# Kernel optimization log

Measured on AMD Instinct MI355X. Metric: run time of the kernel, lower is better.

## Reference

```python
import jax, jax.numpy as jnp
import numpy as np

D_MODEL = 1024
NUM_HEADS = 16
HEAD_SIZE = D_MODEL // NUM_HEADS
THETA = 10000.0
MAX_SEQ_LEN = 4096


def _rope_tables():
    # (max_seq_len, head_size//2) cos/sin tables, matching RotaryPositionalEmbedding
    k = jnp.arange(HEAD_SIZE // 2, dtype=jnp.float32)
    inv_freq = 1.0 / (THETA ** (2.0 * k / HEAD_SIZE))
    pos = jnp.arange(MAX_SEQ_LEN, dtype=jnp.float32)
    ang = pos[:, None] * inv_freq[None, :]
    return jnp.cos(ang), jnp.sin(ang)


def _apply_rope(x, cos, sin):
    # x: (b, h, s, d); cos/sin: (s, d//2) -> broadcast over (b, h)
    x1 = x[..., ::2]
    x2 = x[..., 1::2]
    out_even = x1 * cos - x2 * sin
    out_odd = x2 * cos + x1 * sin
    # re-interleave pairs back to (..., d)
    return jnp.stack([out_even, out_odd], axis=-1).reshape(x.shape)


def setup_inputs() -> dict:
    key = jax.random.key(0)
    k1, k2, k3 = jax.random.split(key, 3)
    b, s = 1, 4096
    std_qkv = np.sqrt(2.0 / (D_MODEL + 3 * D_MODEL))
    std_o = np.sqrt(2.0 / (D_MODEL + D_MODEL))
    return {
        "x": jax.random.normal(k1, (b, s, D_MODEL), dtype=jnp.float32),
        "token_positions": jnp.arange(s, dtype=jnp.int32),
        "W_qkv": jax.random.normal(k2, (3 * D_MODEL, D_MODEL), dtype=jnp.float32) * std_qkv,
        "W_o": jax.random.normal(k3, (D_MODEL, D_MODEL), dtype=jnp.float32) * std_o,
    }


def reference(x, token_positions, W_qkv, W_o):
    b, s, _ = x.shape
    qkv = jnp.einsum("bsd,ed->bse", x, W_qkv)  # (b, s, 3*d_model)
    q, k, v = jnp.split(qkv, 3, axis=-1)

    def to_heads(t):
        return t.reshape(b, s, NUM_HEADS, HEAD_SIZE).transpose(0, 2, 1, 3)  # (b, h, s, hs)

    q, k, v = to_heads(q), to_heads(k), to_heads(v)

    cos_tab, sin_tab = _rope_tables()
    cos = cos_tab[token_positions]  # (s, hs//2)
    sin = sin_tab[token_positions]
    q = _apply_rope(q, cos, sin)
    k = _apply_rope(k, cos, sin)

    scale = 1.0 / jnp.sqrt(jnp.asarray(HEAD_SIZE, dtype=x.dtype))
    scores = jnp.einsum("bhqd,bhkd->bhqk", q, k) * scale  # (b, h, s, s)
    causal = jnp.tril(jnp.ones((s, s), dtype=bool))
    scores = jnp.where(causal, scores, jnp.finfo(scores.dtype).min)
    attn = jax.nn.softmax(scores, axis=-1)
    out = jnp.einsum("bhqk,bhkd->bhqd", attn, v)  # (b, h, s, hs)
    out = out.transpose(0, 2, 1, 3).reshape(b, s, D_MODEL)
    return jnp.einsum("bsd,ed->bse", out, W_o)
```

## Files before the change

### kernel.cpp

```cpp
#include <hip/hip_runtime.h>
#include <stdint.h>

typedef unsigned short u16;
typedef __attribute__((ext_vector_type(8))) short bf16x8;
typedef __attribute__((ext_vector_type(4))) float f32x4;

#define LN_THETA 9.210340371976184f
#define SLEN 4096
#define DMODEL 1024

__device__ __forceinline__ u16 f2bf(float f) {
  union { float f; unsigned u; } v; v.f = f;
  unsigned u = v.u;
  return (u16)((u + 0x7FFFu + ((u >> 16) & 1u)) >> 16);
}
__device__ __forceinline__ u16 f2bf_trunc(float f) {
  union { float f; unsigned u; } v; v.f = f;
  return (u16)(v.u >> 16);
}
__device__ __forceinline__ float bf2f(u16 b) {
  union { unsigned u; float f; } v; v.u = ((unsigned)b) << 16;
  return v.f;
}
__device__ __forceinline__ float fexp2(float x) {
#if __has_builtin(__builtin_amdgcn_exp2f)
  return __builtin_amdgcn_exp2f(x);
#else
  return exp2f(x);
#endif
}

__device__ __forceinline__ f32x4 mfma16(bf16x8 a, bf16x8 b, f32x4 c) {
  return __builtin_amdgcn_mfma_f32_16x16x32_bf16(a, b, c, 0, 0, 0);
}

__device__ __forceinline__ void async16(const u16* g, u16* l) {
  __builtin_amdgcn_global_load_lds(
      (const __attribute__((address_space(1))) unsigned int*)g,
      (__attribute__((address_space(3))) unsigned int*)l, 16, 0, 0);
}

__global__ void prep_kernel(const int* __restrict__ tokpos,
                            float2* __restrict__ tab,
                            const float* __restrict__ x,
                            const float* __restrict__ wqkv,
                            const float* __restrict__ wo,
                            u16* __restrict__ xb, u16* __restrict__ wqkvb,
                            u16* __restrict__ wob) {
  if (blockIdx.x < 512) {
    int t = blockIdx.x * 256 + threadIdx.x;
    int s = t >> 5, i = t & 31;
    float inv = expf(-(float)(2 * i) * (LN_THETA / 64.0f));
    float ang = (float)tokpos[s] * inv;
    float sn, cs;
    sincosf(ang, &sn, &cs);
    tab[t] = make_float2(cs, sn);
    return;
  }
  int i = (blockIdx.x - 512) * 256 + threadIdx.x;
  const float* src;
  u16* dst;
  if (i < (1 << 20)) {
    src = x; dst = xb;
  } else if (i < (1 << 20) + (3 << 18)) {
    i -= (1 << 20); src = wqkv; dst = wqkvb;
  } else {
    i -= (1 << 20) + (3 << 18); src = wo; dst = wob;
  }
  float4 v = ((const float4*)src)[i];
  ushort4 o;
  o.x = f2bf(v.x); o.y = f2bf(v.y); o.z = f2bf(v.z); o.w = f2bf(v.w);
  ((ushort4*)dst)[i] = o;
}

__global__ __launch_bounds__(256) void gemm_qkv_kernel(
    const u16* __restrict__ A, const u16* __restrict__ B,
    u16* __restrict__ qb, u16* __restrict__ kb,
    u16* __restrict__ vbT, const float2* __restrict__ cstab) {
  const int K = 1024;
  __shared__ __align__(16) char smem[128 * 136 * 2];
  u16 (*As)[64] = (u16(*)[64])smem;
  u16 (*Bs)[64] = (u16(*)[64])(smem + 16384);
  u16 (*Ts)[136] = (u16(*)[136])smem;
  const int tid = threadIdx.x;
  const int wave = tid >> 6, lane = tid & 63;
  const int quad = lane >> 4, col = lane & 15;
  const int rowBase = blockIdx.x * 128;
  const int colBase = blockIdx.y * 128;
  const int wm = (wave >> 1) * 64, wn = (wave & 1) * 64;

  const int sr8 = lane >> 3;
  const int sseg = ((lane & 7) ^ sr8) * 8;
  const u16* gA = A + (size_t)(rowBase + wave * 8 + sr8) * K + sseg;
  const u16* gB = B + (size_t)(colBase + wave * 8 + sr8) * K + sseg;
  u16* ldsA = &As[wave * 8 + sr8][(lane & 7) * 8];
  u16* ldsB = &Bs[wave * 8 + sr8][(lane & 7) * 8];

  const int segh[2] = {((quad ^ (col & 7)) * 8), (((4 + quad) ^ (col & 7)) * 8)};

  f32x4 acc[4][4];
#pragma unroll
  for (int i = 0; i < 4; ++i)
#pragma unroll
    for (int j = 0; j < 4; ++j)
      acc[i][j] = f32x4{0.f, 0.f, 0.f, 0.f};

  for (int kk = 0; kk < K; kk += 64) {
    __syncthreads();
#pragma unroll
    for (int j = 0; j < 4; ++j) {
      async16(gA + (size_t)j * 32 * K + kk, ldsA + j * 32 * 64);
      async16(gB + (size_t)j * 32 * K + kk, ldsB + j * 32 * 64);
    }
    __syncthreads();
#pragma unroll
    for (int h = 0; h < 2; ++h) {
      bf16x8 af[4], bfr[4];
#pragma unroll
      for (int i = 0; i < 4; ++i)
        af[i] = *(const bf16x8*)&As[wm + i * 16 + col][segh[h]];
#pragma unroll
      for (int j = 0; j < 4; ++j)
        bfr[j] = *(const bf16x8*)&Bs[wn + j * 16 + col][segh[h]];
#pragma unroll
      for (int i = 0; i < 4; ++i)
#pragma unroll
        for (int j = 0; j < 4; ++j)
          acc[i][j] = mfma16(af[i], bfr[j], acc[i][j]);
    }
  }
  __syncthreads();

  const int sec = rowBase >> 10;

  if (sec < 2) {
    const float qs = (sec == 0) ? 0.125f * 1.4426950408889634f : 1.0f;
#pragma unroll
    for (int j = 0; j < 4; ++j) {
      int sl = wn + j * 16 + col;
      int s = colBase + sl;
#pragma unroll
      for (int i = 0; i < 4; ++i) {
        int el = wm + i * 16 + quad * 4;
        int d = (rowBase + el) & 63;
        float v0 = acc[i][j][0], v1 = acc[i][j][1];
        float v2 = acc[i][j][2], v3 = acc[i][j][3];
        float2 cs0 = cstab[s * 32 + (d >> 1)];
        float2 cs1 = cstab[s * 32 + (d >> 1) + 1];
        ushort4 pk;
        pk.x = f2bf(qs * (v0 * cs0.x - v1 * cs0.y));
        pk.y = f2bf(qs * (v1 * cs0.x + v0 * cs0.y));
        pk.z = f2bf(qs * (v2 * cs1.x - v3 * cs1.y));
        pk.w = f2bf(qs * (v3 * cs1.x + v2 * cs1.y));
        *(ushort4*)&Ts[sl][el] = pk;
      }
    }
    __syncthreads();
    int sl = tid >> 1, hf = tid & 1;
    int hh = ((rowBase & 1023) >> 6) + hf;
    u16* dst = (sec == 0 ? qb : kb) + ((size_t)hh * SLEN + colBase + sl) * 64;
    const u16* srcp = &Ts[sl][hf * 64];
#pragma unroll
    for (int kq = 0; kq < 8; ++kq)
      ((int4*)dst)[kq] = ((const int4*)srcp)[kq];
  } else {
#pragma unroll
    for (int j = 0; j < 4; ++j) {
      int sl = wn + j * 16 + col;
#pragma unroll
      for (int i = 0; i < 4; ++i) {
        int el = wm + i * 16 + quad * 4;
#pragma unroll
        for (int r = 0; r < 4; ++r)
          Ts[el + r][sl] = f2bf(acc[i][j][r]);
      }
    }
    __syncthreads();
    int el = tid >> 1, sh = tid & 1;
    int e = rowBase - 2048 + el;
    int hh = e >> 6, d = e & 63;
    u16* dst = vbT + (size_t)(hh * 64 + d) * SLEN + colBase + sh * 64;
    const u16* srcp = &Ts[el][sh * 64];
#pragma unroll
    for (int kq = 0; kq < 8; ++kq)
      ((int4*)dst)[kq] = ((const int4*)srcp)[kq];
  }
}

__global__ __launch_bounds__(256) void gemm_out_kernel(
    const u16* __restrict__ A, const u16* __restrict__ B,
    float* __restrict__ outf) {
  const int K = 1024;
  __shared__ __align__(16) u16 As[128][64];
  __shared__ __align__(16) u16 Bs[64][64];
  const int tid = threadIdx.x;
  const int wave = tid >> 6, lane = tid & 63;
  const int quad = lane >> 4, col = lane & 15;
  const int rowBase = blockIdx.x * 128;
  const int colBase = blockIdx.y * 64;

  const int sr8 = lane >> 3;
  const int sseg = ((lane & 7) ^ sr8) * 8;
  const u16* gA = A + (size_t)(rowBase + wave * 8 + sr8) * K + sseg;
  const u16* gB = B + (size_t)(colBase + wave * 8 + sr8) * K + sseg;
  u16* ldsA = &As[wave * 8 + sr8][(lane & 7) * 8];
  u16* ldsB = &Bs[wave * 8 + sr8][(lane & 7) * 8];

  const int segh[2] = {((quad ^ (col & 7)) * 8), (((4 + quad) ^ (col & 7)) * 8)};

  f32x4 acc[2][4];
#pragma unroll
  for (int i = 0; i < 2; ++i)
#pragma unroll
    for (int j = 0; j < 4; ++j)
      acc[i][j] = f32x4{0.f, 0.f, 0.f, 0.f};

  for (int kk = 0; kk < K; kk += 64) {
    __syncthreads();
#pragma unroll
    for (int j = 0; j < 4; ++j)
      async16(gA + (size_t)j * 32 * K + kk, ldsA + j * 32 * 64);
#pragma unroll
    for (int j = 0; j < 2; ++j)
      async16(gB + (size_t)j * 32 * K + kk, ldsB + j * 32 * 64);
    __syncthreads();
#pragma unroll
    for (int h = 0; h < 2; ++h) {
      bf16x8 af[2], bfr[4];
#pragma unroll
      for (int i = 0; i < 2; ++i)
        af[i] = *(const bf16x8*)&As[wave * 32 + i * 16 + col][segh[h]];
#pragma unroll
      for (int j = 0; j < 4; ++j)
        bfr[j] = *(const bf16x8*)&Bs[j * 16 + col][segh[h]];
#pragma unroll
      for (int i = 0; i < 2; ++i)
#pragma unroll
        for (int j = 0; j < 4; ++j)
          acc[i][j] = mfma16(af[i], bfr[j], acc[i][j]);
    }
  }

#pragma unroll
  for (int i = 0; i < 2; ++i) {
    int r0 = rowBase + wave * 32 + i * 16 + quad * 4;
#pragma unroll
    for (int j = 0; j < 4; ++j) {
      int cc = colBase + j * 16 + col;
#pragma unroll
      for (int r = 0; r < 4; ++r)
        outf[(size_t)(r0 + r) * DMODEL + cc] = acc[i][j][r];
    }
  }
}

__global__ __launch_bounds__(256) void flash_kernel(
    const u16* __restrict__ qbuf, const u16* __restrict__ kbuf,
    const u16* __restrict__ vbT, u16* __restrict__ po,
    float* __restrict__ pl) {
  const int S = SLEN;
  const int h = blockIdx.x;
  const int y = blockIdx.y;
  int tile, c0, c1;
  if (y < 32) {
    tile = 32 + y; c0 = 0; c1 = 31;
  } else {
    int k = (y - 32) >> 1;
    if ((y - 32) & 1) { tile = 31 - k; c0 = 0; c1 = tile; }
    else { tile = 63 - k; c0 = 32; c1 = tile; }
  }
  const int id = (tile < 32) ? tile : (32 + 2 * (tile - 32) + (c0 ? 1 : 0));

  const int wave = threadIdx.x >> 6, lane = threadIdx.x & 63;
  const int quad = lane >> 4, col = lane & 15;
  const u16* Q = qbuf + (size_t)h * S * 64;
  const u16* Kh = kbuf + (size_t)h * S * 64;
  const u16* Vt = vbT + (size_t)h * 64 * S;

  __shared__ __align__(16) u16 Ks[64][64];
  __shared__ __align__(16) u16 Vs[64][64];
  __shared__ __align__(16) u16 Pld[4][16][72];

  const int sr = lane >> 3;
  const int sw = ((lane & 7) ^ sr) * 8;
  const int dcol = (lane & 7) * 8;
  const int segA = ((quad ^ (col & 7)) * 8);
  const int segB = (((quad ^ 4) ^ (col & 7)) * 8);

  const int qrow0 = tile * 64 + wave * 16;

  bf16x8 qf0, qf1;
  {
    const u16* qp = &Q[(size_t)(qrow0 + col) * 64 + quad * 8];
    qf0 = *(const bf16x8*)qp;
    qf1 = *(const bf16x8*)(qp + 32);
  }

  const bf16x8 ones = {(short)0x3F80, (short)0x3F80, (short)0x3F80,
                       (short)0x3F80, (short)0x3F80, (short)0x3F80,
                       (short)0x3F80, (short)0x3F80};

  f32x4 o[4], lacc;
#pragma unroll
  for (int n = 0; n < 4; ++n) o[n] = f32x4{0.f, 0.f, 0.f, 0.f};
  lacc = f32x4{0.f, 0.f, 0.f, 0.f};

  for (int c = c0; c <= c1; ++c) {
    const int k0 = c * 64;
    __syncthreads();
    {
#pragma unroll
      for (int t = 0; t < 2; ++t) {
        int row = wave * 16 + t * 8 + sr;
        async16(Kh + (size_t)(k0 + row) * 64 + sw, &Ks[row][dcol]);
        async16(Vt + (size_t)row * S + k0 + sw, &Vs[row][dcol]);
      }
    }
    __syncthreads();

    bf16x8 kf0[4], kf1[4], vf0[4], vf1[4];
#pragma unroll
    for (int j = 0; j < 4; ++j) {
      kf0[j] = *(const bf16x8*)&Ks[16 * j + col][segA];
      kf1[j] = *(const bf16x8*)&Ks[16 * j + col][segB];
    }
#pragma unroll
    for (int n = 0; n < 4; ++n) {
      vf0[n] = *(const bf16x8*)&Vs[16 * n + col][segA];
      vf1[n] = *(const bf16x8*)&Vs[16 * n + col][segB];
    }
    const bool lastc = (c == tile);
    f32x4 s[4];
#pragma unroll
    for (int j = 0; j < 4; ++j)
      s[j] = mfma16(qf1, kf1[j],
                    mfma16(qf0, kf0[j], f32x4{0.f, 0.f, 0.f, 0.f}));
    float p[4][4];
#pragma unroll
    for (int r = 0; r < 4; ++r) {
      const int qabs = qrow0 + quad * 4 + r;
#pragma unroll
      for (int j = 0; j < 4; ++j) {
        float e = fexp2(s[j][r]);
        if (lastc && (k0 + 16 * j + col > qabs)) e = 0.f;
        p[j][r] = e;
      }
    }
#pragma unroll
    for (int j = 0; j < 4; ++j)
#pragma unroll
      for (int r = 0; r < 4; ++r)
        Pld[wave][quad * 4 + r][16 * j + col] = f2bf_trunc(p[j][r]);
    bf16x8 pa0 = *(const bf16x8*)&Pld[wave][col][quad * 8];
    bf16x8 pa1 = *(const bf16x8*)&Pld[wave][col][quad * 8 + 32];
    lacc = mfma16(pa1, ones, mfma16(pa0, ones, lacc));
#pragma unroll
    for (int n = 0; n < 4; ++n)
      o[n] = mfma16(pa1, vf1[n], mfma16(pa0, vf0[n], o[n]));
  }

  u16* pob = po + (((size_t)h * 96 + id) * 64) * 64;
  float* plb = pl + ((size_t)h * 96 + id) * 64;
#pragma unroll
  for (int r = 0; r < 4; ++r) {
    int rowl = wave * 16 + quad * 4 + r;
    u16* dst = pob + (size_t)rowl * 64 + col;
#pragma unroll
    for (int n = 0; n < 4; ++n) dst[16 * n] = f2bf(o[n][r]);
    if (col == 0) plb[rowl] = lacc[r];
  }
}

__global__ __launch_bounds__(256) void reduce_kernel(
    const u16* __restrict__ po, const float* __restrict__ pl,
    u16* __restrict__ attn) {
  const int h = blockIdx.x, tile = blockIdx.y;
  const int tid = threadIdx.x;
  const int row = tid >> 2, dg = (tid & 3) * 16;
  int id0, ns;
  if (tile < 32) { id0 = tile; ns = 1; }
  else { id0 = 32 + 2 * (tile - 32); ns = 2; }

  float acc[16];
#pragma unroll
  for (int q = 0; q < 16; ++q) acc[q] = 0.f;
  float l = 0.f;
  for (int s = 0; s < ns; ++s) {
    const size_t base = ((size_t)h * 96 + id0 + s) * 64;
    const u16* p = po + (base + row) * 64 + dg;
    l += pl[base + row];
#pragma unroll
    for (int q = 0; q < 16; ++q) acc[q] += bf2f(p[q]);
  }
  float inv = 1.0f / l;
  u16* dst = attn + (size_t)(tile * 64 + row) * DMODEL + h * 64 + dg;
  ushort4 o0, o1, o2, o3;
  o0.x = f2bf(acc[0] * inv);  o0.y = f2bf(acc[1] * inv);
  o0.z = f2bf(acc[2] * inv);  o0.w = f2bf(acc[3] * inv);
  o1.x = f2bf(acc[4] * inv);  o1.y = f2bf(acc[5] * inv);
  o1.z = f2bf(acc[6] * inv);  o1.w = f2bf(acc[7] * inv);
  o2.x = f2bf(acc[8] * inv);  o2.y = f2bf(acc[9] * inv);
  o2.z = f2bf(acc[10] * inv); o2.w = f2bf(acc[11] * inv);
  o3.x = f2bf(acc[12] * inv); o3.y = f2bf(acc[13] * inv);
  o3.z = f2bf(acc[14] * inv); o3.w = f2bf(acc[15] * inv);
  ((ushort4*)dst)[0] = o0; ((ushort4*)dst)[1] = o1;
  ((ushort4*)dst)[2] = o2; ((ushort4*)dst)[3] = o3;
}

extern "C" void kernel_launch(void* const* d_in, const int* in_sizes, int n_in,
                              void* d_out, int out_size, void* d_ws,
                              size_t ws_size, hipStream_t stream) {
  const float* x = (const float*)d_in[0];
  const int* tokpos = (const int*)d_in[1];
  const float* wqkv = (const float*)d_in[2];
  const float* wo = (const float*)d_in[3];
  float* out = (float*)d_out;

  char* ws = (char*)d_ws;
  u16* xb    = (u16*)(ws);
  u16* wqkvb = (u16*)(ws + ((size_t)8 << 20));
  u16* wob   = (u16*)(ws + ((size_t)14 << 20));
  u16* qb    = (u16*)(ws + ((size_t)16 << 20));
  u16* kb    = (u16*)(ws + ((size_t)24 << 20));
  u16* vbT   = (u16*)(ws + ((size_t)32 << 20));
  u16* attn  = (u16*)(ws + ((size_t)40 << 20));
  float2* cstab = (float2*)(ws + ((size_t)48 << 20));
  u16* po    = (u16*)(ws);
  float* pl  = (float*)(ws + ((size_t)13 << 20));

  prep_kernel<<<dim3(8704), dim3(256), 0, stream>>>(tokpos, cstab, x, wqkv, wo,
                                                    xb, wqkvb, wob);
  gemm_qkv_kernel<<<dim3(24, 32), dim3(256), 0, stream>>>(
      wqkvb, xb, qb, kb, vbT, cstab);
  flash_kernel<<<dim3(16, 96), dim3(256), 0, stream>>>(qb, kb, vbT, po, pl);
  reduce_kernel<<<dim3(16, 64), dim3(256), 0, stream>>>(po, pl, attn);
  gemm_out_kernel<<<dim3(32, 16), dim3(256), 0, stream>>>(attn, wob, out);
}
```

Before: 210.4 us.

## Shrink GEMM tiles for more blocks and transpose flash scores for packed P stores

Both GEMM kernels switch to smaller output tiles (QKV 128x64, out-projection 64x64) and double their grids, so more blocks run across the CUs and each thread holds fewer registers. The flash kernel computes scores transposed (K times Q), so each lane holds consecutive keys for one query row. It can then write P to LDS as packed bf16 pairs using a byte-permute instead of scattered 16-bit stores. The smaller tiles lower per-block data reuse and add global traffic in exchange for more parallelism.

```diff
diff --git a/kernel.cpp b/kernel.cpp
--- a/kernel.cpp
+++ b/kernel.cpp
@@ -13,10 +13,6 @@
   union { float f; unsigned u; } v; v.f = f;
   unsigned u = v.u;
   return (u16)((u + 0x7FFFu + ((u >> 16) & 1u)) >> 16);
-}
-__device__ __forceinline__ u16 f2bf_trunc(float f) {
-  union { float f; unsigned u; } v; v.f = f;
-  return (u16)(v.u >> 16);
 }
 __device__ __forceinline__ float bf2f(u16 b) {
   union { unsigned u; float f; } v; v.u = ((unsigned)b) << 16;
@@ -27,6 +23,15 @@
   return __builtin_amdgcn_exp2f(x);
 #else
   return exp2f(x);
+#endif
+}
+__device__ __forceinline__ unsigned pack_bf16_trunc(float lo, float hi) {
+  union { float f; unsigned u; } a, b;
+  a.f = hi; b.f = lo;
+#if __has_builtin(__builtin_amdgcn_perm)
+  return __builtin_amdgcn_perm(a.u, b.u, 0x07060302u);
+#else
+  return (a.u & 0xffff0000u) | (b.u >> 16);
 #endif
 }
 
@@ -78,16 +83,17 @@
     u16* __restrict__ qb, u16* __restrict__ kb,
     u16* __restrict__ vbT, const float2* __restrict__ cstab) {
   const int K = 1024;
-  __shared__ __align__(16) char smem[128 * 136 * 2];
+  __shared__ __align__(16) char smem[24576];
   u16 (*As)[64] = (u16(*)[64])smem;
   u16 (*Bs)[64] = (u16(*)[64])(smem + 16384);
   u16 (*Ts)[136] = (u16(*)[136])smem;
+  u16 (*Tv)[72]  = (u16(*)[72])smem;
   const int tid = threadIdx.x;
   const int wave = tid >> 6, lane = tid & 63;
   const int quad = lane >> 4, col = lane & 15;
   const int rowBase = blockIdx.x * 128;
-  const int colBase = blockIdx.y * 128;
-  const int wm = (wave >> 1) * 64, wn = (wave & 1) * 64;
+  const int colBase = blockIdx.y * 64;
+  const int wm = wave * 32;
 
   const int sr8 = lane >> 3;
   const int sseg = ((lane & 7) ^ sr8) * 8;
@@ -98,9 +104,9 @@
 
   const int segh[2] = {((quad ^ (col & 7)) * 8), (((4 + quad) ^ (col & 7)) * 8)};
 
-  f32x4 acc[4][4];
-#pragma unroll
-  for (int i = 0; i < 4; ++i)
+  f32x4 acc[2][4];
+#pragma unroll
+  for (int i = 0; i < 2; ++i)
 #pragma unroll
     for (int j = 0; j < 4; ++j)
       acc[i][j] = f32x4{0.f, 0.f, 0.f, 0.f};
@@ -108,22 +114,23 @@
   for (int kk = 0; kk < K; kk += 64) {
     __syncthreads();
 #pragma unroll
-    for (int j = 0; j < 4; ++j) {
-      async16(gA + (size_t)j * 32 * K + kk, ldsA + j * 32 * 64);
-      async16(gB + (size_t)j * 32 * K + kk, ldsB + j * 32 * 64);
-    }
+    for (int t = 0; t < 4; ++t)
+      async16(gA + (size_t)t * 32 * K + kk, ldsA + t * 32 * 64);
+#pragma unroll
+    for (int t = 0; t < 2; ++t)
+      async16(gB + (size_t)t * 32 * K + kk, ldsB + t * 32 * 64);
     __syncthreads();
 #pragma unroll
     for (int h = 0; h < 2; ++h) {
-      bf16x8 af[4], bfr[4];
-#pragma unroll
-      for (int i = 0; i < 4; ++i)
+      bf16x8 af[2], bfr[4];
+#pragma unroll
+      for (int i = 0; i < 2; ++i)
         af[i] = *(const bf16x8*)&As[wm + i * 16 + col][segh[h]];
 #pragma unroll
       for (int j = 0; j < 4; ++j)
-        bfr[j] = *(const bf16x8*)&Bs[wn + j * 16 + col][segh[h]];
-#pragma unroll
-      for (int i = 0; i < 4; ++i)
+        bfr[j] = *(const bf16x8*)&Bs[j * 16 + col][segh[h]];
+#pragma unroll
+      for (int i = 0; i < 2; ++i)
 #pragma unroll
         for (int j = 0; j < 4; ++j)
           acc[i][j] = mfma16(af[i], bfr[j], acc[i][j]);
@@ -137,10 +144,10 @@
     const float qs = (sec == 0) ? 0.125f * 1.4426950408889634f : 1.0f;
 #pragma unroll
     for (int j = 0; j < 4; ++j) {
-      int sl = wn + j * 16 + col;
+      int sl = j * 16 + col;
       int s = colBase + sl;
 #pragma unroll
-      for (int i = 0; i < 4; ++i) {
+      for (int i = 0; i < 2; ++i) {
         int el = wm + i * 16 + quad * 4;
         int d = (rowBase + el) & 63;
         float v0 = acc[i][j][0], v1 = acc[i][j][1];
@@ -156,33 +163,35 @@
       }
     }
     __syncthreads();
-    int sl = tid >> 1, hf = tid & 1;
-    int hh = ((rowBase & 1023) >> 6) + hf;
-    u16* dst = (sec == 0 ? qb : kb) + ((size_t)hh * SLEN + colBase + sl) * 64;
-    const u16* srcp = &Ts[sl][hf * 64];
-#pragma unroll
-    for (int kq = 0; kq < 8; ++kq)
+    int sl = tid >> 2, ec = tid & 3;
+    int hh = ((rowBase & 1023) >> 6) + (ec >> 1);
+    int d0 = (ec & 1) * 32;
+    u16* dst = (sec == 0 ? qb : kb) +
+               ((size_t)hh * SLEN + colBase + sl) * 64 + d0;
+    const u16* srcp = &Ts[sl][ec * 32];
+#pragma unroll
+    for (int kq = 0; kq < 4; ++kq)
       ((int4*)dst)[kq] = ((const int4*)srcp)[kq];
   } else {
 #pragma unroll
     for (int j = 0; j < 4; ++j) {
-      int sl = wn + j * 16 + col;
-#pragma unroll
-      for (int i = 0; i < 4; ++i) {
+      int sl = j * 16 + col;
+#pragma unroll
+      for (int i = 0; i < 2; ++i) {
         int el = wm + i * 16 + quad * 4;
 #pragma unroll
         for (int r = 0; r < 4; ++r)
-          Ts[el + r][sl] = f2bf(acc[i][j][r]);
+          Tv[el + r][sl] = f2bf(acc[i][j][r]);
       }
     }
     __syncthreads();
-    int el = tid >> 1, sh = tid & 1;
+    int el = tid >> 1, sc = tid & 1;
     int e = rowBase - 2048 + el;
     int hh = e >> 6, d = e & 63;
-    u16* dst = vbT + (size_t)(hh * 64 + d) * SLEN + colBase + sh * 64;
-    const u16* srcp = &Ts[el][sh * 64];
-#pragma unroll
-    for (int kq = 0; kq < 8; ++kq)
+    u16* dst = vbT + (size_t)(hh * 64 + d) * SLEN + colBase + sc * 32;
+    const u16* srcp = &Tv[el][sc * 32];
+#pragma unroll
+    for (int kq = 0; kq < 4; ++kq)
       ((int4*)dst)[kq] = ((const int4*)srcp)[kq];
   }
 }
@@ -191,12 +200,12 @@
     const u16* __restrict__ A, const u16* __restrict__ B,
     float* __restrict__ outf) {
   const int K = 1024;
-  __shared__ __align__(16) u16 As[128][64];
+  __shared__ __align__(16) u16 As[64][64];
   __shared__ __align__(16) u16 Bs[64][64];
   const int tid = threadIdx.x;
   const int wave = tid >> 6, lane = tid & 63;
   const int quad = lane >> 4, col = lane & 15;
-  const int rowBase = blockIdx.x * 128;
+  const int rowBase = blockIdx.x * 64;
   const int colBase = blockIdx.y * 64;
 
   const int sr8 = lane >> 3;
@@ -208,49 +217,38 @@
 
   const int segh[2] = {((quad ^ (col & 7)) * 8), (((4 + quad) ^ (col & 7)) * 8)};
 
-  f32x4 acc[2][4];
-#pragma unroll
-  for (int i = 0; i < 2; ++i)
-#pragma unroll
-    for (int j = 0; j < 4; ++j)
-      acc[i][j] = f32x4{0.f, 0.f, 0.f, 0.f};
+  f32x4 acc[4];
+#pragma unroll
+  for (int j = 0; j < 4; ++j) acc[j] = f32x4{0.f, 0.f, 0.f, 0.f};
 
   for (int kk = 0; kk < K; kk += 64) {
     __syncthreads();
 #pragma unroll
-    for (int j = 0; j < 4; ++j)
-      async16(gA + (size_t)j * 32 * K + kk, ldsA + j * 32 * 64);
-#pragma unroll
-    for (int j = 0; j < 2; ++j)
-      async16(gB + (size_t)j * 32 * K + kk, ldsB + j * 32 * 64);
+    for (int t = 0; t < 2; ++t) {
+      async16(gA + (size_t)t * 32 * K + kk, ldsA + t * 32 * 64);
+      async16(gB + (size_t)t * 32 * K + kk, ldsB + t * 32 * 64);
+    }
     __syncthreads();
 #pragma unroll
     for (int h = 0; h < 2; ++h) {
-      bf16x8 af[2], bfr[4];
-#pragma unroll
-      for (int i = 0; i < 2; ++i)
-        af[i] = *(const bf16x8*)&As[wave * 32 + i * 16 + col][segh[h]];
+      bf16x8 af = *(const bf16x8*)&As[wave * 16 + col][segh[h]];
+      bf16x8 bfr[4];
 #pragma unroll
       for (int j = 0; j < 4; ++j)
         bfr[j] = *(const bf16x8*)&Bs[j * 16 + col][segh[h]];
 #pragma unroll
-      for (int i = 0; i < 2; ++i)
-#pragma unroll
-        for (int j = 0; j < 4; ++j)
-          acc[i][j] = mfma16(af[i], bfr[j], acc[i][j]);
-    }
-  }
-
-#pragma unroll
-  for (int i = 0; i < 2; ++i) {
-    int r0 = rowBase + wave * 32 + i * 16 + quad * 4;
-#pragma unroll
-    for (int j = 0; j < 4; ++j) {
-      int cc = colBase + j * 16 + col;
-#pragma unroll
-      for (int r = 0; r < 4; ++r)
-        outf[(size_t)(r0 + r) * DMODEL + cc] = acc[i][j][r];
-    }
+      for (int j = 0; j < 4; ++j)
+        acc[j] = mfma16(af, bfr[j], acc[j]);
+    }
+  }
+
+  int r0 = rowBase + wave * 16 + quad * 4;
+#pragma unroll
+  for (int j = 0; j < 4; ++j) {
+    int cc = colBase + j * 16 + col;
+#pragma unroll
+    for (int r = 0; r < 4; ++r)
+      outf[(size_t)(r0 + r) * DMODEL + cc] = acc[j][r];
   }
 }
 
@@ -288,6 +286,7 @@
   const int segB = (((quad ^ 4) ^ (col & 7)) * 8);
 
   const int qrow0 = tile * 64 + wave * 16;
+  const int wcol = wave * 16 + col;
 
   bf16x8 qf0, qf1;
   {
@@ -330,27 +329,27 @@
       vf1[n] = *(const bf16x8*)&Vs[16 * n + col][segB];
     }
     const bool lastc = (c == tile);
-    f32x4 s[4];
-#pragma unroll
-    for (int j = 0; j < 4; ++j)
-      s[j] = mfma16(qf1, kf1[j],
-                    mfma16(qf0, kf0[j], f32x4{0.f, 0.f, 0.f, 0.f}));
+    f32x4 st[4];
+#pragma unroll
+    for (int jb = 0; jb < 4; ++jb)
+      st[jb] = mfma16(kf1[jb], qf1,
+                      mfma16(kf0[jb], qf0, f32x4{0.f, 0.f, 0.f, 0.f}));
     float p[4][4];
 #pragma unroll
-    for (int r = 0; r < 4; ++r) {
-      const int qabs = qrow0 + quad * 4 + r;
-#pragma unroll
-      for (int j = 0; j < 4; ++j) {
-        float e = fexp2(s[j][r]);
-        if (lastc && (k0 + 16 * j + col > qabs)) e = 0.f;
-        p[j][r] = e;
+    for (int jb = 0; jb < 4; ++jb)
+#pragma unroll
+      for (int r = 0; r < 4; ++r) {
+        float e = fexp2(st[jb][r]);
+        if (lastc && (16 * jb + quad * 4 + r > wcol)) e = 0.f;
+        p[jb][r] = e;
       }
-    }
-#pragma unroll
-    for (int j = 0; j < 4; ++j)
-#pragma unroll
-      for (int r = 0; r < 4; ++r)
-        Pld[wave][quad * 4 + r][16 * j + col] = f2bf_trunc(p[j][r]);
+#pragma unroll
+    for (int jb = 0; jb < 4; ++jb)
+#pragma unroll
+      for (int u = 0; u < 2; ++u) {
+        unsigned pk = pack_bf16_trunc(p[jb][2 * u], p[jb][2 * u + 1]);
+        *(unsigned*)&Pld[wave][col][16 * jb + quad * 4 + 2 * u] = pk;
+      }
     bf16x8 pa0 = *(const bf16x8*)&Pld[wave][col][quad * 8];
     bf16x8 pa1 = *(const bf16x8*)&Pld[wave][col][quad * 8 + 32];
     lacc = mfma16(pa1, ones, mfma16(pa0, ones, lacc));
@@ -430,9 +429,9 @@
 
   prep_kernel<<<dim3(8704), dim3(256), 0, stream>>>(tokpos, cstab, x, wqkv, wo,
                                                     xb, wqkvb, wob);
-  gemm_qkv_kernel<<<dim3(24, 32), dim3(256), 0, stream>>>(
+  gemm_qkv_kernel<<<dim3(24, 64), dim3(256), 0, stream>>>(
       wqkvb, xb, qb, kb, vbT, cstab);
   flash_kernel<<<dim3(16, 96), dim3(256), 0, stream>>>(qb, kb, vbT, po, pl);
   reduce_kernel<<<dim3(16, 64), dim3(256), 0, stream>>>(po, pl, attn);
-  gemm_out_kernel<<<dim3(32, 16), dim3(256), 0, stream>>>(attn, wob, out);
-}
+  gemm_out_kernel<<<dim3(64, 16), dim3(256), 0, stream>>>(attn, wob, out);
+}
```

After: 204.6 us. 1.03x faster.
